# Kernel optimization log

Hardware: AMD Instinct MI355X
Metric: run time of the kernel (lower is better)

## Reference

```python
import jax, jax.numpy as jnp
import numpy as np

# config (matches init_kwargs)
B, L, Q = 4, 2048, 2048      # batch, memory_length, query_len
H, D = 16, 64                # heads, head_dim
E = H * D                    # hidden_dim = 1024
NB = 512                     # num_basis
SIGMAS = np.array([0.005, 0.01])
RIDGE = 0.5
CLAMP_MIN = 1e-4


def _build_basis():
    # torch.meshgrid(linspace(0,1,NB//2), sigmas) then flatten: mu repeated, sigma tiled
    mu = np.repeat(np.linspace(0.0, 1.0, NB // len(SIGMAS)), len(SIGMAS))
    sg = np.tile(SIGMAS, NB // len(SIGMAS))
    return mu, sg


def _build_G(mu, sg):
    # get_positions(L, padding=True), L even: 2L points in [-0.5+shift, 1.5-shift]
    shift = 1.0 / (2 * L)
    pos = np.linspace(-0.5 + shift, 1.5 - shift, 2 * L)
    # F[j, p] = N(pos_p; mu_j, sg_j)
    Fm = np.exp(-0.5 * ((pos[None, :] - mu[:, None]) / sg[:, None]) ** 2) / (sg[:, None] * np.sqrt(2 * np.pi))
    G = Fm.T @ np.linalg.inv(Fm @ Fm.T + RIDGE * np.eye(NB))  # [2L, NB]
    return G[L // 2:-(L // 2)]  # [L, NB]


def setup_inputs() -> dict:
    key = jax.random.key(0)
    ks = jax.random.split(key, 8)
    mu, sg = _build_basis()
    G = _build_G(mu, sg)
    s_e = 1.0 / np.sqrt(E)
    s_n = 1.0 / np.sqrt(NB)
    return {
        "k": jax.random.normal(ks[0], (B, L, E), jnp.float32),
        "q": jax.random.normal(ks[1], (B, Q, E), jnp.float32),
        "Wq": jax.random.normal(ks[2], (E, E), jnp.float32) * s_e,
        "Wk": jax.random.normal(ks[3], (E, E), jnp.float32) * s_e,
        "Wv": jax.random.normal(ks[4], (E, E), jnp.float32) * s_e,
        "Wo": jax.random.normal(ks[5], (E, E), jnp.float32) * s_e,
        "w_mu": jax.random.normal(ks[6], (NB,), jnp.float32) * s_n,
        "w_sigma": jax.random.normal(ks[7], (NB,), jnp.float32) * s_n,
        "Gs": jnp.asarray(G, jnp.float32),
        "basis_mu": jnp.asarray(mu, jnp.float32),
        "basis_sigma": jnp.asarray(sg, jnp.float32),
    }


def reference(k, q, Wq, Wk, Wv, Wo, w_mu, w_sigma, Gs, basis_mu, basis_sigma):
    # continuous compression of the memory: B_mat[b,n,e] = sum_l k[b,l,e] * Gs[l,n]
    Bm = jnp.einsum('ble,ln->bne', k, Gs)  # [B, NB, E]
    keys = (Bm @ Wk.T).reshape(B, NB, H, D).transpose(0, 2, 1, 3)   # [B,H,NB,D]
    vals = (Bm @ Wv.T).reshape(B, NB, H, D).transpose(0, 2, 1, 3)   # [B,H,NB,D]
    qry = (q @ Wq.T).reshape(B, Q, H, D).transpose(0, 2, 1, 3)      # [B,H,Q,D]
    # scores over basis functions
    scores = jnp.einsum('bhqd,bhnd->bhqn', qry, keys) / jnp.sqrt(jnp.float32(D))
    # affine heads -> Gaussian attention density parameters per query
    mu_q = jax.nn.sigmoid(scores @ w_mu)[..., None]                         # [B,H,Q,1]
    sig2 = jnp.clip(jax.nn.softplus(scores @ w_sigma), CLAMP_MIN)[..., None]  # [B,H,Q,1]
    # continuous softmax closed form: r_j = N(mu_q; basis_mu_j, sig2 + basis_sigma_j^2)
    var = sig2 + basis_sigma ** 2                                           # [B,H,Q,NB]
    r = jnp.exp(-0.5 * (mu_q - basis_mu) ** 2 / var) / jnp.sqrt(2.0 * jnp.pi * var)
    ctx = jnp.einsum('bhqn,bhnd->bhqd', r, vals)                            # [B,H,Q,D]
    ctx = ctx.transpose(0, 2, 1, 3).reshape(B, Q, E)
    return ctx @ Wo.T
```

## Files before the change

kernel.cpp:

```cpp
#include <hip/hip_runtime.h>

#define BB 4
#define LL 2048
#define QQ 2048
#define HH 16
#define DD 64
#define EE 1024
#define NB 512

typedef __attribute__((ext_vector_type(8))) short bf16x8;
typedef __attribute__((ext_vector_type(4))) float f32x4;

__device__ inline ushort bf16_rne(float f) {
  uint u = __float_as_uint(f);
  return (ushort)((u + 0x7fffu + ((u >> 16) & 1u)) >> 16);
}
__device__ inline float bf16_f(ushort h) { return __uint_as_float((uint)h << 16); }
__device__ inline void hilo(float x, ushort& h, ushort& l) {
  h = bf16_rne(x);
  l = bf16_rne(x - bf16_f(h));
}

__device__ inline void cvt8_pack(const float* a, uint4& ph, uint4& pl) {
  ushort h[8], l[8];
  #pragma unroll
  for (int j = 0; j < 8; j++) hilo(a[j], h[j], l[j]);
  ph = make_uint4((uint)h[0] | ((uint)h[1] << 16), (uint)h[2] | ((uint)h[3] << 16),
                  (uint)h[4] | ((uint)h[5] << 16), (uint)h[6] | ((uint)h[7] << 16));
  pl = make_uint4((uint)l[0] | ((uint)l[1] << 16), (uint)l[2] | ((uint)l[3] << 16),
                  (uint)l[4] | ((uint)l[5] << 16), (uint)l[6] | ((uint)l[7] << 16));
}

__global__ __launch_bounds__(256) void cvt_hilo(
    const float* __restrict__ x, ushort* __restrict__ hi, ushort* __restrict__ lo, long n)
{
  long i0 = ((long)blockIdx.x * 256 + threadIdx.x) * 8;
  long stride = (long)gridDim.x * 2048;
  for (long i = i0; i < n; i += stride) {
    float a[8];
    *(float4*)&a[0] = *(const float4*)&x[i];
    *(float4*)&a[4] = *(const float4*)&x[i + 4];
    uint4 ph, pl;
    cvt8_pack(a, ph, pl);
    *(uint4*)&hi[i] = ph;
    *(uint4*)&lo[i] = pl;
  }
}

__global__ __launch_bounds__(256) void cvt_hiloT(
    const float* __restrict__ x, ushort* __restrict__ hiT, ushort* __restrict__ loT,
    int R, int C, long zIn, long zOut)
{
  x += (long)blockIdx.z * zIn; hiT += (long)blockIdx.z * zOut; loT += (long)blockIdx.z * zOut;
  __shared__ float tile[32][33];
  const int t = threadIdx.x;
  const long r0 = (long)blockIdx.y * 32, c0 = (long)blockIdx.x * 32;
  {
    int row = t >> 3, c4 = t & 7;
    float4 v = *(const float4*)&x[(r0 + row) * C + c0 + c4 * 4];
    tile[row][c4*4+0] = v.x; tile[row][c4*4+1] = v.y;
    tile[row][c4*4+2] = v.z; tile[row][c4*4+3] = v.w;
  }
  __syncthreads();
  {
    int col = t >> 3, r4 = t & 7;
    ushort h[4], l[4];
    #pragma unroll
    for (int j = 0; j < 4; j++) hilo(tile[r4 * 4 + j][col], h[j], l[j]);
    uint2 ph = make_uint2((uint)h[0] | ((uint)h[1] << 16), (uint)h[2] | ((uint)h[3] << 16));
    uint2 pl = make_uint2((uint)l[0] | ((uint)l[1] << 16), (uint)l[2] | ((uint)l[3] << 16));
    long o = (c0 + col) * (long)R + r0 + r4 * 4;
    *(uint2*)&hiT[o] = ph;
    *(uint2*)&loT[o] = pl;
  }
}

__global__ __launch_bounds__(256) void add_pairs(
    float* __restrict__ dst, long dstStride,
    const float* __restrict__ src, long srcPairStride, long n)
{
  float* d = dst + (long)blockIdx.z * dstStride;
  const float* s0 = src + (long)blockIdx.z * srcPairStride;
  const float* s1 = s0 + n;
  long i0 = ((long)blockIdx.x * 256 + threadIdx.x) * 4;
  long stride = (long)gridDim.x * 1024;
  for (long i = i0; i < n; i += stride) {
    float4 a = *(const float4*)&s0[i];
    float4 b = *(const float4*)&s1[i];
    a.x += b.x; a.y += b.y; a.z += b.z; a.w += b.w;
    *(float4*)&d[i] = a;
  }
}


__global__ __launch_bounds__(256) void gemm_nt128(
    const float* __restrict__ A, const float* __restrict__ B, float* __restrict__ C,
    int N, int K, long sA, long sB, long sC, int NS, int Kc)
{
  const int z = blockIdx.z;
  const int b = z / NS, ks = z - b * NS;
  A += (long)b * sA + (long)ks * Kc;
  B += (long)b * sB + (long)ks * Kc;
  C += (long)z * sC;
  __shared__ float As[32][132], Bs[32][132];
  const int t = threadIdx.x;
  const int tx = t & 15, ty = t >> 4;
  const long m0 = (long)blockIdx.y * 128, n0 = (long)blockIdx.x * 128;
  float acc[8][8] = {};
  for (int k0 = 0; k0 < Kc; k0 += 32) {
    #pragma unroll
    for (int i = 0; i < 4; i++) {
      int f = t + i * 256;
      int r = f >> 3, k4 = f & 7;
      float4 va = *(const float4*)&A[(m0 + r) * K + k0 + k4 * 4];
      As[k4*4+0][r] = va.x; As[k4*4+1][r] = va.y; As[k4*4+2][r] = va.z; As[k4*4+3][r] = va.w;
      float4 vb = *(const float4*)&B[(n0 + r) * K + k0 + k4 * 4];
      Bs[k4*4+0][r] = vb.x; Bs[k4*4+1][r] = vb.y; Bs[k4*4+2][r] = vb.z; Bs[k4*4+3][r] = vb.w;
    }
    __syncthreads();
    #pragma unroll
    for (int kk = 0; kk < 32; kk++) {
      float4 a0 = *(const float4*)&As[kk][ty*8];
      float4 a1 = *(const float4*)&As[kk][ty*8+4];
      float4 b0 = *(const float4*)&Bs[kk][tx*8];
      float4 b1 = *(const float4*)&Bs[kk][tx*8+4];
      float ar[8] = {a0.x,a0.y,a0.z,a0.w,a1.x,a1.y,a1.z,a1.w};
      float br[8] = {b0.x,b0.y,b0.z,b0.w,b1.x,b1.y,b1.z,b1.w};
      #pragma unroll
      for (int i = 0; i < 8; i++)
        #pragma unroll
        for (int j = 0; j < 8; j++)
          acc[i][j] += ar[i] * br[j];
    }
    __syncthreads();
  }
  #pragma unroll
  for (int i = 0; i < 8; i++) {
    float4 o0 = make_float4(acc[i][0], acc[i][1], acc[i][2], acc[i][3]);
    float4 o1 = make_float4(acc[i][4], acc[i][5], acc[i][6], acc[i][7]);
    *(float4*)&C[(m0 + ty*8 + i) * N + n0 + tx*8    ] = o0;
    *(float4*)&C[(m0 + ty*8 + i) * N + n0 + tx*8 + 4] = o1;
  }
}

__global__ __launch_bounds__(256) void gemm_tn128(
    const float* __restrict__ A, const float* __restrict__ B, float* __restrict__ C,
    int M, int N, long sA, long sB, long sC, int NS, int Kc)
{
  const int z = blockIdx.z;
  const int b = z / NS, ks = z - b * NS;
  A += (long)b * sA + (long)ks * Kc * M;
  B += (long)b * sB + (long)ks * Kc * N;
  C += (long)z * sC;
  __shared__ float As[32][132], Bs[32][132];
  const int t = threadIdx.x;
  const int tx = t & 15, ty = t >> 4;
  const long m0 = (long)blockIdx.y * 128, n0 = (long)blockIdx.x * 128;
  float acc[8][8] = {};
  for (int k0 = 0; k0 < Kc; k0 += 32) {
    #pragma unroll
    for (int i = 0; i < 4; i++) {
      int f = t + i * 256;
      int r = f >> 5, c4 = f & 31;
      *(float4*)&As[r][c4 * 4] = *(const float4*)&A[(long)(k0 + r) * M + m0 + c4 * 4];
      *(float4*)&Bs[r][c4 * 4] = *(const float4*)&B[(long)(k0 + r) * N + n0 + c4 * 4];
    }
    __syncthreads();
    #pragma unroll
    for (int kk = 0; kk < 32; kk++) {
      float4 a0 = *(const float4*)&As[kk][ty*8];
      float4 a1 = *(const float4*)&As[kk][ty*8+4];
      float4 b0 = *(const float4*)&Bs[kk][tx*8];
      float4 b1 = *(const float4*)&Bs[kk][tx*8+4];
      float ar[8] = {a0.x,a0.y,a0.z,a0.w,a1.x,a1.y,a1.z,a1.w};
      float br[8] = {b0.x,b0.y,b0.z,b0.w,b1.x,b1.y,b1.z,b1.w};
      #pragma unroll
      for (int i = 0; i < 8; i++)
        #pragma unroll
        for (int j = 0; j < 8; j++)
          acc[i][j] += ar[i] * br[j];
    }
    __syncthreads();
  }
  #pragma unroll
  for (int i = 0; i < 8; i++) {
    float4 o0 = make_float4(acc[i][0], acc[i][1], acc[i][2], acc[i][3]);
    float4 o1 = make_float4(acc[i][4], acc[i][5], acc[i][6], acc[i][7]);
    *(float4*)&C[(m0 + ty*8 + i) * N + n0 + tx*8    ] = o0;
    *(float4*)&C[(m0 + ty*8 + i) * N + n0 + tx*8 + 4] = o1;
  }
}

__global__ __launch_bounds__(256) void gemm_nt64(
    const float* __restrict__ A, const float* __restrict__ B, float* __restrict__ C,
    int M, int N, int K, long sA, long sB, long sC)
{
  A += (long)blockIdx.z * sA; B += (long)blockIdx.z * sB; C += (long)blockIdx.z * sC;
  __shared__ float As[32][68], Bs[32][68];
  const int t = threadIdx.x;
  const int tx = t & 15, ty = t >> 4;
  const int m0 = blockIdx.y * 64, n0 = blockIdx.x * 64;
  float acc[4][4] = {};
  for (int k0 = 0; k0 < K; k0 += 32) {
    #pragma unroll
    for (int i = 0; i < 2; i++) {
      int f = t + i * 256;
      int r = f >> 3, k4 = f & 7;
      float4 va = *(const float4*)&A[(long)(m0 + r) * K + k0 + k4 * 4];
      As[k4*4+0][r] = va.x; As[k4*4+1][r] = va.y; As[k4*4+2][r] = va.z; As[k4*4+3][r] = va.w;
      float4 vb = *(const float4*)&B[(long)(n0 + r) * K + k0 + k4 * 4];
      Bs[k4*4+0][r] = vb.x; Bs[k4*4+1][r] = vb.y; Bs[k4*4+2][r] = vb.z; Bs[k4*4+3][r] = vb.w;
    }
    __syncthreads();
    #pragma unroll
    for (int kk = 0; kk < 32; kk++) {
      float4 a4 = *(const float4*)&As[kk][ty * 4];
      float4 b4 = *(const float4*)&Bs[kk][tx * 4];
      float ar[4] = {a4.x, a4.y, a4.z, a4.w};
      float br[4] = {b4.x, b4.y, b4.z, b4.w};
      #pragma unroll
      for (int i = 0; i < 4; i++)
        #pragma unroll
        for (int j = 0; j < 4; j++)
          acc[i][j] += ar[i] * br[j];
    }
    __syncthreads();
  }
  #pragma unroll
  for (int i = 0; i < 4; i++) {
    float4 o = make_float4(acc[i][0], acc[i][1], acc[i][2], acc[i][3]);
    *(float4*)&C[(long)(m0 + ty*4 + i) * N + n0 + tx*4] = o;
  }
}


__global__ __launch_bounds__(256) void gemm_nt128_b3(
    const ushort* __restrict__ Ah, const ushort* __restrict__ Al,
    const ushort* __restrict__ Bh, const ushort* __restrict__ Bl,
    float* __restrict__ C, int N, int K, long sA, long sC, int NS, int Kc)
{
  const int z = blockIdx.z;
  const int zb = z / NS, ks = z - zb * NS;
  Ah += (long)zb * sA + (long)ks * Kc;
  Al += (long)zb * sA + (long)ks * Kc;
  Bh += (long)ks * Kc;
  Bl += (long)ks * Kc;
  C  += (long)z * sC;
  __shared__ ushort AhS[4096], AlS[4096], BhS[4096], BlS[4096];
  const int t = threadIdx.x;
  const int l = t & 63, w = t >> 6;
  const long m0 = (long)blockIdx.y * 128, n0 = (long)blockIdx.x * 128;
  const int frA = (w & 1) * 4;
  const int frB = (w >> 1) * 4;
  f32x4 acc[4][4] = {};
  for (int k0 = 0; k0 < Kc; k0 += 32) {
    #pragma unroll
    for (int p = 0; p < 2; p++) {
      int t2 = t + p * 256;
      int row = t2 >> 2, kq = t2 & 3;
      long goff = (m0 + row) * (long)K + k0 + kq * 8;
      long gofB = (n0 + row) * (long)K + k0 + kq * 8;
      int dst = (row >> 4) * 512 + ((row & 15) + 16 * kq) * 8;
      *(uint4*)&AhS[dst] = *(const uint4*)(Ah + goff);
      *(uint4*)&AlS[dst] = *(const uint4*)(Al + goff);
      *(uint4*)&BhS[dst] = *(const uint4*)(Bh + gofB);
      *(uint4*)&BlS[dst] = *(const uint4*)(Bl + gofB);
    }
    __syncthreads();
    bf16x8 ah[4], al[4], bh[4], bl[4];
    #pragma unroll
    for (int i = 0; i < 4; i++) {
      ah[i] = *(const bf16x8*)&AhS[(frA + i) * 512 + l * 8];
      al[i] = *(const bf16x8*)&AlS[(frA + i) * 512 + l * 8];
      bh[i] = *(const bf16x8*)&BhS[(frB + i) * 512 + l * 8];
      bl[i] = *(const bf16x8*)&BlS[(frB + i) * 512 + l * 8];
    }
    #pragma unroll
    for (int i = 0; i < 4; i++)
      #pragma unroll
      for (int j = 0; j < 4; j++) {
        acc[i][j] = __builtin_amdgcn_mfma_f32_16x16x32_bf16(ah[i], bh[j], acc[i][j], 0, 0, 0);
        acc[i][j] = __builtin_amdgcn_mfma_f32_16x16x32_bf16(ah[i], bl[j], acc[i][j], 0, 0, 0);
        acc[i][j] = __builtin_amdgcn_mfma_f32_16x16x32_bf16(al[i], bh[j], acc[i][j], 0, 0, 0);
      }
    __syncthreads();
  }
  const long rbase = m0 + (w & 1) * 64 + (l >> 4) * 4;
  const int  cbase = (int)n0 + (w >> 1) * 64 + (l & 15);
  #pragma unroll
  for (int i = 0; i < 4; i++)
    #pragma unroll
    for (int j = 0; j < 4; j++)
      #pragma unroll
      for (int r = 0; r < 4; r++)
        C[(rbase + i * 16 + r) * N + cbase + j * 16] = acc[i][j][r];
}

__global__ __launch_bounds__(256) void gemm_nt64x128_b3(
    const ushort* __restrict__ Ah, const ushort* __restrict__ Al,
    const ushort* __restrict__ Bh, const ushort* __restrict__ Bl,
    float* __restrict__ C, int N, int K, long sB, long sC)
{
  const int z = blockIdx.z;
  Bh += (long)z * sB; Bl += (long)z * sB; C += (long)z * sC;
  __shared__ ushort AhS[2048], AlS[2048], BhS[4096], BlS[4096];
  const int t = threadIdx.x;
  const int l = t & 63, w = t >> 6;
  const long m0 = (long)blockIdx.y * 64, n0 = (long)blockIdx.x * 128;
  const int wm = w & 1, wn = w >> 1;
  f32x4 acc[2][4] = {};
  for (int k0 = 0; k0 < K; k0 += 32) {
    {
      int row = t >> 2, kq = t & 3;
      long goff = (m0 + row) * (long)K + k0 + kq * 8;
      int dst = (row >> 4) * 512 + ((row & 15) + 16 * kq) * 8;
      *(uint4*)&AhS[dst] = *(const uint4*)(Ah + goff);
      *(uint4*)&AlS[dst] = *(const uint4*)(Al + goff);
    }
    #pragma unroll
    for (int p = 0; p < 2; p++) {
      int t2 = t + p * 256;
      int row = t2 >> 2, kq = t2 & 3;
      long gofB = (n0 + row) * (long)K + k0 + kq * 8;
      int dst = (row >> 4) * 512 + ((row & 15) + 16 * kq) * 8;
      *(uint4*)&BhS[dst] = *(const uint4*)(Bh + gofB);
      *(uint4*)&BlS[dst] = *(const uint4*)(Bl + gofB);
    }
    __syncthreads();
    bf16x8 ah[2], al[2], bh[4], bl[4];
    #pragma unroll
    for (int i = 0; i < 2; i++) {
      ah[i] = *(const bf16x8*)&AhS[(wm * 2 + i) * 512 + l * 8];
      al[i] = *(const bf16x8*)&AlS[(wm * 2 + i) * 512 + l * 8];
    }
    #pragma unroll
    for (int j = 0; j < 4; j++) {
      bh[j] = *(const bf16x8*)&BhS[(wn * 4 + j) * 512 + l * 8];
      bl[j] = *(const bf16x8*)&BlS[(wn * 4 + j) * 512 + l * 8];
    }
    #pragma unroll
    for (int i = 0; i < 2; i++)
      #pragma unroll
      for (int j = 0; j < 4; j++) {
        acc[i][j] = __builtin_amdgcn_mfma_f32_16x16x32_bf16(ah[i], bh[j], acc[i][j], 0, 0, 0);
        acc[i][j] = __builtin_amdgcn_mfma_f32_16x16x32_bf16(ah[i], bl[j], acc[i][j], 0, 0, 0);
        acc[i][j] = __builtin_amdgcn_mfma_f32_16x16x32_bf16(al[i], bh[j], acc[i][j], 0, 0, 0);
      }
    __syncthreads();
  }
  const long rbase = m0 + wm * 32 + (l >> 4) * 4;
  const int  cbase = (int)n0 + wn * 64 + (l & 15);
  #pragma unroll
  for (int i = 0; i < 2; i++)
    #pragma unroll
    for (int j = 0; j < 4; j++)
      #pragma unroll
      for (int r = 0; r < 4; r++)
        C[(rbase + i * 16 + r) * N + cbase + j * 16] = acc[i][j][r];
}

__global__ __launch_bounds__(256) void cvt_valsT(
    const float* __restrict__ valsP, ushort* __restrict__ vTh, ushort* __restrict__ vTl,
    long slabStride)
{
  const int c = blockIdx.x, h = blockIdx.y, b = blockIdx.z;
  const int t = threadIdx.x;
  __shared__ float tile[32][68];
  const float* s0 = valsP + (long)(2 * b) * slabStride;
  const float* s1 = s0 + slabStride;
  {
    int r = t >> 3, c8 = (t & 7) * 8;
    long g = (long)(c * 32 + r) * EE + h * 64 + c8;
    float4 a0 = *(const float4*)&s0[g];     float4 b0 = *(const float4*)&s1[g];
    float4 a1 = *(const float4*)&s0[g + 4]; float4 b1 = *(const float4*)&s1[g + 4];
    a0.x += b0.x; a0.y += b0.y; a0.z += b0.z; a0.w += b0.w;
    a1.x += b1.x; a1.y += b1.y; a1.z += b1.z; a1.w += b1.w;
    *(float4*)&tile[r][c8] = a0;
    *(float4*)&tile[r][c8 + 4] = a1;
  }
  __syncthreads();
  const int f = t >> 6, l = t & 63;
  const int d = f * 16 + (l & 15), kq = l >> 4;
  float a[8];
  #pragma unroll
  for (int e = 0; e < 8; e++) a[e] = tile[kq * 8 + e][d];
  uint4 ph, pl;
  cvt8_pack(a, ph, pl);
  long obase = (((long)(b * HH + h) * 16 + c) * 2048) + (long)t * 8;
  *(uint4*)&vTh[obase] = ph;
  *(uint4*)&vTl[obase] = pl;
}

__global__ __launch_bounds__(256) void nb_ctx_mf(
    const ushort* __restrict__ vTh, const ushort* __restrict__ vTl,
    const float* __restrict__ muq, const float* __restrict__ sg2,
    const float* __restrict__ bmu, const float* __restrict__ bsg,
    ushort* __restrict__ ctxh, ushort* __restrict__ ctxl,
    long sMu, long sC)
{
  const int h = blockIdx.y, b = blockIdx.z;
  const long q0 = (long)blockIdx.x * 128;
  const int t = threadIdx.x;
  const int l = t & 63, w = t >> 6, wm = w & 1, wn = w >> 1;
  __shared__ ushort AhS[4096], AlS[4096];
  __shared__ ushort BhS[2048], BlS[2048];
  __shared__ float mu_s[128], s2_s[128], bm_s[NB], bv_s[NB];
  const float* muqb = muq + (long)b * sMu;
  const float* sg2b = sg2 + (long)b * sMu;
  if (t < 128) {
    mu_s[t] = muqb[(long)h * QQ + q0 + t];
    s2_s[t] = sg2b[(long)h * QQ + q0 + t];
  }
  for (int i = t; i < NB; i += 256) {
    bm_s[i] = bmu[i];
    float x = bsg[i];
    bv_s[i] = x * x;
  }
  __syncthreads();
  const ushort* vThb = vTh + ((long)(b * HH + h) * 16) * 2048;
  const ushort* vTlb = vTl + ((long)(b * HH + h) * 16) * 2048;
  f32x4 acc[4][2] = {};
  for (int c = 0; c < 16; c++) {
    ((uint4*)BhS)[t] = ((const uint4*)(vThb + c * 2048))[t];
    ((uint4*)BlS)[t] = ((const uint4*)(vTlb + c * 2048))[t];
    #pragma unroll
    for (int p = 0; p < 2; p++) {
      int s = t + p * 256;
      int lf = s & 63;
      int q = ((s >> 6) << 4) + (lf & 15);
      int nb = c * 32 + (lf >> 4) * 8;
      float m = mu_s[q], s2 = s2_s[q];
      float a[8];
      #pragma unroll
      for (int e = 0; e < 8; e++) {
        float v = s2 + bv_s[nb + e];
        float d = m - bm_s[nb + e];
        float rv = __builtin_amdgcn_rcpf(v);
        a[e] = __expf(d * d * rv * -0.5f) * __builtin_amdgcn_rsqf(v * 6.2831853071795865f);
      }
      uint4 ph, pl;
      cvt8_pack(a, ph, pl);
      *(uint4*)&AhS[s * 8] = ph;
      *(uint4*)&AlS[s * 8] = pl;
    }
    __syncthreads();
    bf16x8 bhf[2], blf[2];
    #pragma unroll
    for (int j = 0; j < 2; j++) {
      bhf[j] = *(const bf16x8*)&BhS[(wn * 2 + j) * 512 + l * 8];
      blf[j] = *(const bf16x8*)&BlS[(wn * 2 + j) * 512 + l * 8];
    }
    #pragma unroll
    for (int i = 0; i < 4; i++) {
      bf16x8 ah = *(const bf16x8*)&AhS[(wm * 4 + i) * 512 + l * 8];
      bf16x8 al = *(const bf16x8*)&AlS[(wm * 4 + i) * 512 + l * 8];
      #pragma unroll
      for (int j = 0; j < 2; j++) {
        acc[i][j] = __builtin_amdgcn_mfma_f32_16x16x32_bf16(ah, bhf[j], acc[i][j], 0, 0, 0);
        acc[i][j] = __builtin_amdgcn_mfma_f32_16x16x32_bf16(ah, blf[j], acc[i][j], 0, 0, 0);
        acc[i][j] = __builtin_amdgcn_mfma_f32_16x16x32_bf16(al, bhf[j], acc[i][j], 0, 0, 0);
      }
    }
    __syncthreads();
  }
  ushort* ch = ctxh + (long)b * sC;
  ushort* cl = ctxl + (long)b * sC;
  const long rbase = q0 + wm * 64 + (l >> 4) * 4;
  const int  cbase = h * 64 + wn * 32 + (l & 15);
  #pragma unroll
  for (int i = 0; i < 4; i++)
    #pragma unroll
    for (int j = 0; j < 2; j++)
      #pragma unroll
      for (int r = 0; r < 4; r++) {
        long off = (rbase + i * 16 + r) * EE + cbase + j * 16;
        ushort hb, lb;
        hilo(acc[i][j][r], hb, lb);
        ch[off] = hb;
        cl[off] = lb;
      }
}

__global__ __launch_bounds__(256) void nb_uvec(
    const float* __restrict__ Bm, const float* __restrict__ wmu, const float* __restrict__ wsg,
    float* __restrict__ ump, float* __restrict__ usp, long sBm, long sU)
{
  Bm += (long)blockIdx.z * sBm; ump += (long)blockIdx.z * sU; usp += (long)blockIdx.z * sU;
  const int e = blockIdx.x * 256 + threadIdx.x;
  const int c = blockIdx.y;
  float am = 0.f, as = 0.f;
  #pragma unroll 8
  for (int n = c * 64; n < c * 64 + 64; n++) {
    float bv = Bm[(long)n * EE + e];
    am += wmu[n] * bv;
    as += wsg[n] * bv;
  }
  ump[(long)c * EE + e] = am;
  usp[(long)c * EE + e] = as;
}

__global__ __launch_bounds__(256) void nb_kw(
    const float* __restrict__ Wk, const float* __restrict__ ump, const float* __restrict__ usp,
    float* __restrict__ kwm, float* __restrict__ kws, long sU, long sK)
{
  ump += (long)blockIdx.z * sU; usp += (long)blockIdx.z * sU;
  kwm += (long)blockIdx.z * sK; kws += (long)blockIdx.z * sK;
  __shared__ float pm[256], ps[256];
  const int e = blockIdx.x, t = threadIdx.x;
  const float* row = Wk + (long)e * EE;
  float am = 0.f, as = 0.f;
  for (int i = t; i < EE; i += 256) {
    float um = 0.f, us = 0.f;
    #pragma unroll
    for (int c = 0; c < 8; c++) { um += ump[(long)c * EE + i]; us += usp[(long)c * EE + i]; }
    float w = row[i];
    am += w * um;
    as += w * us;
  }
  pm[t] = am; ps[t] = as;
  __syncthreads();
  for (int s = 128; s > 0; s >>= 1) {
    if (t < s) { pm[t] += pm[t + s]; ps[t] += ps[t + s]; }
    __syncthreads();
  }
  if (t == 0) { kwm[e] = pm[0]; kws[e] = ps[0]; }
}

__global__ __launch_bounds__(256) void nb_amas(
    const float* __restrict__ Wq, const float* __restrict__ kwm, const float* __restrict__ kws,
    float* __restrict__ AmAs, long sK, long sAm)
{
  kwm += (long)blockIdx.z * sK; kws += (long)blockIdx.z * sK;
  AmAs += (long)blockIdx.z * sAm;
  __shared__ float km[64], ks[64];
  const int t = threadIdx.x;
  const int h = blockIdx.y;
  const int e = blockIdx.x * 256 + t;
  if (t < 64) { km[t] = kwm[h * 64 + t]; ks[t] = kws[h * 64 + t]; }
  __syncthreads();
  float am = 0.f, as = 0.f;
  #pragma unroll 8
  for (int d = 0; d < 64; d++) {
    float w = Wq[(long)(h * 64 + d) * EE + e];
    am += km[d] * w;
    as += ks[d] * w;
  }
  AmAs[(long)e * 32 + h]      = am;
  AmAs[(long)e * 32 + 16 + h] = as;
}

__global__ __launch_bounds__(256) void nb_musig(
    const float* __restrict__ qb, const float* __restrict__ AmAs,
    float* __restrict__ muq, float* __restrict__ sg2, long sQ, long sAm, long sMu)
{
  qb += (long)blockIdx.z * sQ; AmAs += (long)blockIdx.z * sAm;
  muq += (long)blockIdx.z * sMu; sg2 += (long)blockIdx.z * sMu;
  __shared__ float qs[EE];
  __shared__ float part[8][32];
  const int t = threadIdx.x, qrow = blockIdx.x;
  for (int i = t; i < EE; i += 256) qs[i] = qb[(long)qrow * EE + i];
  __syncthreads();
  const int o = t & 31, ch = t >> 5;
  float acc = 0.f;
  const int e0 = ch * 128;
  #pragma unroll 8
  for (int i = 0; i < 128; i++) {
    int e = e0 + i;
    acc += qs[e] * AmAs[(long)e * 32 + o];
  }
  part[ch][o] = acc;
  __syncthreads();
  if (t < 32) {
    float s = 0.f;
    #pragma unroll
    for (int c = 0; c < 8; c++) s += part[c][o];
    s *= 0.125f;
    if (o < 16) {
      muq[(long)o * QQ + qrow] = 1.f / (1.f + expf(-s));
    } else {
      float sp = (s > 20.f) ? s : log1pf(expf(s));
      sg2[(long)(o - 16) * QQ + qrow] = fmaxf(sp, 1e-4f);
    }
  }
}

__global__ __launch_bounds__(128) void nb_ctx128(
    const float* __restrict__ vals, const float* __restrict__ muq, const float* __restrict__ sg2,
    const float* __restrict__ bmu,  const float* __restrict__ bsg, float* __restrict__ ctx,
    long sV, long sMu, long sC)
{
  vals += (long)blockIdx.z * sV; ctx += (long)blockIdx.z * sC;
  muq += (long)blockIdx.z * sMu; sg2 += (long)blockIdx.z * sMu;
  __shared__ float As[32][132], Bs[32][68];
  __shared__ __align__(16) float mu_s[128], s2_s[128];
  const int t = threadIdx.x;
  const int tx = t & 7, ty = t >> 3;
  const long q0 = (long)blockIdx.x * 128;
  const int h = blockIdx.y;
  mu_s[t] = muq[(long)h * QQ + q0 + t];
  s2_s[t] = sg2[(long)h * QQ + q0 + t];
  __syncthreads();
  float acc[8][8] = {};
  for (int n0 = 0; n0 < NB; n0 += 32) {
    #pragma unroll
    for (int i = 0; i < 4; i++) {
      int f = t + i * 128;
      int r = f >> 4, c4 = f & 15;
      *(float4*)&Bs[r][c4 * 4] = *(const float4*)&vals[(long)(n0 + r) * EE + h * 64 + c4 * 4];
    }
    #pragma unroll
    for (int i = 0; i < 8; i++) {
      int idx = t + i * 128;
      int n = idx >> 5, qg = idx & 31;
      float bm = bmu[n0 + n], bs = bsg[n0 + n];
      float bs2 = bs * bs;
      float4 m4 = *(const float4*)&mu_s[qg * 4];
      float4 s4 = *(const float4*)&s2_s[qg * 4];
      float4 rr;
      {
        float v0 = s4.x + bs2, d0 = m4.x - bm;
        float v1 = s4.y + bs2, d1 = m4.y - bm;
        float v2 = s4.z + bs2, d2 = m4.z - bm;
        float v3 = s4.w + bs2, d3 = m4.w - bm;
        float r0 = __builtin_amdgcn_rcpf(v0), r1 = __builtin_amdgcn_rcpf(v1);
        float r2 = __builtin_amdgcn_rcpf(v2), r3 = __builtin_amdgcn_rcpf(v3);
        rr.x = __expf(d0 * d0 * r0 * -0.5f) * __builtin_amdgcn_rsqf(v0 * 6.2831853071795865f);
        rr.y = __expf(d1 * d1 * r1 * -0.5f) * __builtin_amdgcn_rsqf(v1 * 6.2831853071795865f);
        rr.z = __expf(d2 * d2 * r2 * -0.5f) * __builtin_amdgcn_rsqf(v2 * 6.2831853071795865f);
        rr.w = __expf(d3 * d3 * r3 * -0.5f) * __builtin_amdgcn_rsqf(v3 * 6.2831853071795865f);
      }
      *(float4*)&As[n][qg * 4] = rr;
    }
    __syncthreads();
    #pragma unroll
    for (int kk = 0; kk < 32; kk++) {
      float4 a0 = *(const float4*)&As[kk][ty*8];
      float4 a1 = *(const float4*)&As[kk][ty*8+4];
      float4 b0 = *(const float4*)&Bs[kk][tx*8];
      float4 b1 = *(const float4*)&Bs[kk][tx*8+4];
      float ar[8] = {a0.x,a0.y,a0.z,a0.w,a1.x,a1.y,a1.z,a1.w};
      float br[8] = {b0.x,b0.y,b0.z,b0.w,b1.x,b1.y,b1.z,b1.w};
      #pragma unroll
      for (int i = 0; i < 8; i++)
        #pragma unroll
        for (int j = 0; j < 8; j++)
          acc[i][j] += ar[i] * br[j];
    }
    __syncthreads();
  }
  #pragma unroll
  for (int i = 0; i < 8; i++) {
    float4 o0 = make_float4(acc[i][0], acc[i][1], acc[i][2], acc[i][3]);
    float4 o1 = make_float4(acc[i][4], acc[i][5], acc[i][6], acc[i][7]);
    *(float4*)&ctx[(q0 + ty*8 + i) * EE + h * 64 + tx*8    ] = o0;
    *(float4*)&ctx[(q0 + ty*8 + i) * EE + h * 64 + tx*8 + 4] = o1;
  }
}

extern "C" void kernel_launch(void* const* d_in, const int* in_sizes, int n_in,
                              void* d_out, int out_size, void* d_ws, size_t ws_size,
                              hipStream_t stream) {
  const float* k   = (const float*)d_in[0];
  const float* q   = (const float*)d_in[1];
  const float* Wq  = (const float*)d_in[2];
  const float* Wk  = (const float*)d_in[3];
  const float* Wv  = (const float*)d_in[4];
  const float* Wo  = (const float*)d_in[5];
  const float* wmu = (const float*)d_in[6];
  const float* wsg = (const float*)d_in[7];
  const float* Gs  = (const float*)d_in[8];
  const float* bmu = (const float*)d_in[9];
  const float* bsg = (const float*)d_in[10];
  float* out = (float*)d_out;
  char* ws = (char*)d_ws;

  const long sBm = (long)NB * EE;
  const long sU  = 8L * EE;
  const long sK  = EE;
  const long sAm = 32L * EE;
  const long sMu = (long)HH * QQ;
  const long sQ  = (long)QQ * EE;

  if (ws_size >= (50u << 20)) {
    ushort* kTh  = (ushort*)(ws + 0);
    ushort* kTl  = (ushort*)(ws + (16u << 20));
    ushort* GsTh = (ushort*)(ws + (32u << 20));
    ushort* GsTl = (ushort*)(ws + (34u << 20));
    float*  Bm4  = (float*)(ws + (40u << 20));
    ushort* Bmh  = (ushort*)(ws + 0);
    ushort* Bml  = (ushort*)(ws + (4u << 20));
    ushort* Wvh  = (ushort*)(ws + (8u << 20));
    ushort* Wvl  = (ushort*)(ws + (10u << 20));
    float*  valsP= (float*)(ws + (16u << 20));
    ushort* vTh  = (ushort*)(ws + (32u << 20));
    ushort* vTl  = (ushort*)(ws + (36u << 20));
    ushort* Woh  = (ushort*)(ws + (40u << 20));
    ushort* Wol  = (ushort*)(ws + (42u << 20));
    ushort* ctxh = (ushort*)(ws + 0);
    ushort* ctxl = (ushort*)(ws + (16u << 20));
    char*  sm    = ws + (48u << 20);
    float* ump4  = (float*)(sm);
    float* usp4  = (float*)(sm + (128u << 10));
    float* kwm4  = (float*)(sm + (256u << 10));
    float* kws4  = (float*)(sm + (272u << 10));
    float* AmAs4 = (float*)(sm + (288u << 10));
    float* muq4  = (float*)(sm + (800u << 10));
    float* sg24  = (float*)(sm + (1312u << 10));

    cvt_hiloT<<<dim3(NB/32, LL/32, 1),  256, 0, stream>>>(Gs, GsTh, GsTl, LL, NB, 0L, 0L);
    cvt_hiloT<<<dim3(EE/32, LL/32, BB), 256, 0, stream>>>(k, kTh, kTl, LL, EE,
                                                          (long)LL*EE, (long)LL*EE);
    gemm_nt64x128_b3<<<dim3(EE/128, NB/64, BB), 256, 0, stream>>>(
        GsTh, GsTl, kTh, kTl, Bm4, EE, LL, (long)LL*EE, sBm);
    nb_uvec  <<<dim3(EE/256, 8, BB),  256, 0, stream>>>(Bm4, wmu, wsg, ump4, usp4, sBm, sU);
    nb_kw    <<<dim3(EE, 1, BB),      256, 0, stream>>>(Wk, ump4, usp4, kwm4, kws4, sU, sK);
    nb_amas  <<<dim3(EE/256, HH, BB), 256, 0, stream>>>(Wq, kwm4, kws4, AmAs4, sK, sAm);
    nb_musig <<<dim3(QQ, 1, BB),      256, 0, stream>>>(q, AmAs4, muq4, sg24, sQ, sAm, sMu);
    cvt_hilo<<<dim3(256), 256, 0, stream>>>(Bm4, Bmh, Bml, (long)BB * sBm);
    cvt_hilo<<<dim3(256), 256, 0, stream>>>(Wv, Wvh, Wvl, (long)EE * EE);
    gemm_nt128_b3<<<dim3(EE/128, NB/128, BB*2), 256, 0, stream>>>(
        Bmh, Bml, Wvh, Wvl, valsP, EE, EE, sBm, sBm, 2, EE/2);
    cvt_valsT<<<dim3(16, HH, BB), 256, 0, stream>>>(valsP, vTh, vTl, sBm);
    cvt_hilo<<<dim3(256), 256, 0, stream>>>(Wo, Woh, Wol, (long)EE * EE);
    nb_ctx_mf<<<dim3(QQ/128, HH, BB), 256, 0, stream>>>(
        vTh, vTl, muq4, sg24, bmu, bsg, ctxh, ctxl, sMu, sQ);
    gemm_nt128_b3<<<dim3(EE/128, QQ/128, BB), 256, 0, stream>>>(
        ctxh, ctxl, Woh, Wol, out, EE, EE, sQ, sQ, 1, EE);
  } else {
    float* BmP   = (float*)(ws + 0);
    float* ctxS  = (float*)(ws + 0);
    float* vals4 = (float*)(ws + (16u << 20));
    char*  sm    = ws + (24u << 20);
    float* ump4  = (float*)(sm);
    float* usp4  = (float*)(sm + (128u << 10));
    float* kwm4  = (float*)(sm + (256u << 10));
    float* kws4  = (float*)(sm + (272u << 10));
    float* AmAs4 = (float*)(sm + (288u << 10));
    float* muq4  = (float*)(sm + (800u << 10));
    float* sg24  = (float*)(sm + (1312u << 10));

    gemm_tn128<<<dim3(EE/128, NB/128, BB*2), 256, 0, stream>>>(
        Gs, k, BmP, NB, EE, 0L, (long)LL*EE, sBm, 2, LL/2);
    add_pairs<<<dim3(256, 1, BB), 256, 0, stream>>>(BmP, 2*sBm, BmP, 2*sBm, sBm);
    gemm_nt128<<<dim3(EE/128, NB/128, BB), 256, 0, stream>>>(
        BmP, Wv, vals4, EE, EE, 2*sBm, 0L, sBm, 1, EE);
    nb_uvec  <<<dim3(EE/256, 8, BB),  256, 0, stream>>>(BmP, wmu, wsg, ump4, usp4, 2*sBm, sU);
    nb_kw    <<<dim3(EE, 1, BB),      256, 0, stream>>>(Wk, ump4, usp4, kwm4, kws4, sU, sK);
    nb_amas  <<<dim3(EE/256, HH, BB), 256, 0, stream>>>(Wq, kwm4, kws4, AmAs4, sK, sAm);
    nb_musig <<<dim3(QQ, 1, BB),      256, 0, stream>>>(q, AmAs4, muq4, sg24, sQ, sAm, sMu);
    for (int b = 0; b < BB; b++) {
      nb_ctx128<<<dim3(QQ/128, HH, 1), 128, 0, stream>>>(
          vals4 + (long)b*sBm, muq4 + (long)b*sMu, sg24 + (long)b*sMu,
          bmu, bsg, ctxS, 0L, 0L, 0L);
      gemm_nt64<<<dim3(EE/64, QQ/64, 1), 256, 0, stream>>>(
          ctxS, Wo, out + (long)b*sQ, QQ, EE, EE, 0L, 0L, 0L);
    }
  }
  (void)in_sizes; (void)n_in; (void)out_size;
}
```

Measured before the change: 435.0 us.

## Swizzle GEMM LDS layout, batch musig rows, merge Wv/Wo conversion launches

Three independent changes. The LDS tiles in both split-bf16 GEMM kernels are now stored with an XOR swizzle on the row index, keyed by the k-quarter, and fragment reads use the matching swizzled offset, so LDS bank conflicts on stores and reads should drop. The mu/sigma projection kernel now processes 8 query rows per block, so each AmAs load serves eight rows instead of one, at the cost of 32KB of shared memory per block. The two separate Wv and Wo hi/lo conversion launches are merged into one two-slice launch to save a kernel launch.

```diff
diff --git a/kernel.cpp b/kernel.cpp
--- a/kernel.cpp
+++ b/kernel.cpp
@@ -47,6 +47,26 @@
   }
 }
 
+__global__ __launch_bounds__(256) void cvt_hilo2(
+    const float* __restrict__ x0, ushort* __restrict__ h0, ushort* __restrict__ l0,
+    const float* __restrict__ x1, ushort* __restrict__ h1, ushort* __restrict__ l1, long n)
+{
+  const float* x = blockIdx.y ? x1 : x0;
+  ushort* hi = blockIdx.y ? h1 : h0;
+  ushort* lo = blockIdx.y ? l1 : l0;
+  long i0 = ((long)blockIdx.x * 256 + threadIdx.x) * 8;
+  long stride = (long)gridDim.x * 2048;
+  for (long i = i0; i < n; i += stride) {
+    float a[8];
+    *(float4*)&a[0] = *(const float4*)&x[i];
+    *(float4*)&a[4] = *(const float4*)&x[i + 4];
+    uint4 ph, pl;
+    cvt8_pack(a, ph, pl);
+    *(uint4*)&hi[i] = ph;
+    *(uint4*)&lo[i] = pl;
+  }
+}
+
 __global__ __launch_bounds__(256) void cvt_hiloT(
     const float* __restrict__ x, ushort* __restrict__ hiT, ushort* __restrict__ loT,
     int R, int C, long zIn, long zOut)
@@ -252,6 +272,7 @@
   const long m0 = (long)blockIdx.y * 128, n0 = (long)blockIdx.x * 128;
   const int frA = (w & 1) * 4;
   const int frB = (w >> 1) * 4;
+  const int rs = ((((l & 15) ^ ((l >> 4) << 2)) + 16 * (l >> 4))) * 8;
   f32x4 acc[4][4] = {};
   for (int k0 = 0; k0 < Kc; k0 += 32) {
     #pragma unroll
@@ -260,7 +281,7 @@
       int row = t2 >> 2, kq = t2 & 3;
       long goff = (m0 + row) * (long)K + k0 + kq * 8;
       long gofB = (n0 + row) * (long)K + k0 + kq * 8;
-      int dst = (row >> 4) * 512 + ((row & 15) + 16 * kq) * 8;
+      int dst = (row >> 4) * 512 + ((((row & 15) ^ (kq << 2)) + 16 * kq)) * 8;
       *(uint4*)&AhS[dst] = *(const uint4*)(Ah + goff);
       *(uint4*)&AlS[dst] = *(const uint4*)(Al + goff);
       *(uint4*)&BhS[dst] = *(const uint4*)(Bh + gofB);
@@ -270,10 +291,10 @@
     bf16x8 ah[4], al[4], bh[4], bl[4];
     #pragma unroll
     for (int i = 0; i < 4; i++) {
-      ah[i] = *(const bf16x8*)&AhS[(frA + i) * 512 + l * 8];
-      al[i] = *(const bf16x8*)&AlS[(frA + i) * 512 + l * 8];
-      bh[i] = *(const bf16x8*)&BhS[(frB + i) * 512 + l * 8];
-      bl[i] = *(const bf16x8*)&BlS[(frB + i) * 512 + l * 8];
+      ah[i] = *(const bf16x8*)&AhS[(frA + i) * 512 + rs];
+      al[i] = *(const bf16x8*)&AlS[(frA + i) * 512 + rs];
+      bh[i] = *(const bf16x8*)&BhS[(frB + i) * 512 + rs];
+      bl[i] = *(const bf16x8*)&BlS[(frB + i) * 512 + rs];
     }
     #pragma unroll
     for (int i = 0; i < 4; i++)
@@ -308,12 +329,13 @@
   const int l = t & 63, w = t >> 6;
   const long m0 = (long)blockIdx.y * 64, n0 = (long)blockIdx.x * 128;
   const int wm = w & 1, wn = w >> 1;
+  const int rs = ((((l & 15) ^ ((l >> 4) << 2)) + 16 * (l >> 4))) * 8;
   f32x4 acc[2][4] = {};
   for (int k0 = 0; k0 < K; k0 += 32) {
     {
       int row = t >> 2, kq = t & 3;
       long goff = (m0 + row) * (long)K + k0 + kq * 8;
-      int dst = (row >> 4) * 512 + ((row & 15) + 16 * kq) * 8;
+      int dst = (row >> 4) * 512 + ((((row & 15) ^ (kq << 2)) + 16 * kq)) * 8;
       *(uint4*)&AhS[dst] = *(const uint4*)(Ah + goff);
       *(uint4*)&AlS[dst] = *(const uint4*)(Al + goff);
     }
@@ -322,7 +344,7 @@
       int t2 = t + p * 256;
       int row = t2 >> 2, kq = t2 & 3;
       long gofB = (n0 + row) * (long)K + k0 + kq * 8;
-      int dst = (row >> 4) * 512 + ((row & 15) + 16 * kq) * 8;
+      int dst = (row >> 4) * 512 + ((((row & 15) ^ (kq << 2)) + 16 * kq)) * 8;
       *(uint4*)&BhS[dst] = *(const uint4*)(Bh + gofB);
       *(uint4*)&BlS[dst] = *(const uint4*)(Bl + gofB);
     }
@@ -330,13 +352,13 @@
     bf16x8 ah[2], al[2], bh[4], bl[4];
     #pragma unroll
     for (int i = 0; i < 2; i++) {
-      ah[i] = *(const bf16x8*)&AhS[(wm * 2 + i) * 512 + l * 8];
-      al[i] = *(const bf16x8*)&AlS[(wm * 2 + i) * 512 + l * 8];
+      ah[i] = *(const bf16x8*)&AhS[(wm * 2 + i) * 512 + rs];
+      al[i] = *(const bf16x8*)&AlS[(wm * 2 + i) * 512 + rs];
     }
     #pragma unroll
     for (int j = 0; j < 4; j++) {
-      bh[j] = *(const bf16x8*)&BhS[(wn * 4 + j) * 512 + l * 8];
-      bl[j] = *(const bf16x8*)&BlS[(wn * 4 + j) * 512 + l * 8];
+      bh[j] = *(const bf16x8*)&BhS[(wn * 4 + j) * 512 + rs];
+      bl[j] = *(const bf16x8*)&BlS[(wn * 4 + j) * 512 + rs];
     }
     #pragma unroll
     for (int i = 0; i < 2; i++)
@@ -547,6 +569,33 @@
   }
   AmAs[(long)e * 32 + h]      = am;
   AmAs[(long)e * 32 + 16 + h] = as;
+}
+
+__global__ __launch_bounds__(256) void nb_musig8(
+    const float* __restrict__ qb, const float* __restrict__ AmAs,
+    float* __restrict__ muq, float* __restrict__ sg2, long sQ, long sAm, long sMu)
+{
+  qb += (long)blockIdx.z * sQ; AmAs += (long)blockIdx.z * sAm;
+  muq += (long)blockIdx.z * sMu; sg2 += (long)blockIdx.z * sMu;
+  __shared__ float qs[8 * EE];
+  const int t = threadIdx.x;
+  const long q0 = (long)blockIdx.x * 8;
+  for (int i = t * 4; i < 8 * EE; i += 1024)
+    *(float4*)&qs[i] = *(const float4*)&qb[q0 * EE + i];
+  __syncthreads();
+  const int o = t & 31, row = t >> 5;
+  const float* qr = qs + row * EE;
+  float acc = 0.f;
+  #pragma unroll 8
+  for (int e = 0; e < EE; e++)
+    acc += qr[e] * AmAs[(long)e * 32 + o];
+  float s = acc * 0.125f;
+  if (o < 16) {
+    muq[(long)o * QQ + q0 + row] = 1.f / (1.f + expf(-s));
+  } else {
+    float sp = (s > 20.f) ? s : log1pf(expf(s));
+    sg2[(long)(o - 16) * QQ + q0 + row] = fmaxf(sp, 1e-4f);
+  }
 }
 
 __global__ __launch_bounds__(256) void nb_musig(
@@ -715,13 +764,12 @@
     nb_uvec  <<<dim3(EE/256, 8, BB),  256, 0, stream>>>(Bm4, wmu, wsg, ump4, usp4, sBm, sU);
     nb_kw    <<<dim3(EE, 1, BB),      256, 0, stream>>>(Wk, ump4, usp4, kwm4, kws4, sU, sK);
     nb_amas  <<<dim3(EE/256, HH, BB), 256, 0, stream>>>(Wq, kwm4, kws4, AmAs4, sK, sAm);
-    nb_musig <<<dim3(QQ, 1, BB),      256, 0, stream>>>(q, AmAs4, muq4, sg24, sQ, sAm, sMu);
+    nb_musig8<<<dim3(QQ/8, 1, BB),    256, 0, stream>>>(q, AmAs4, muq4, sg24, sQ, sAm, sMu);
     cvt_hilo<<<dim3(256), 256, 0, stream>>>(Bm4, Bmh, Bml, (long)BB * sBm);
-    cvt_hilo<<<dim3(256), 256, 0, stream>>>(Wv, Wvh, Wvl, (long)EE * EE);
+    cvt_hilo2<<<dim3(128, 2), 256, 0, stream>>>(Wv, Wvh, Wvl, Wo, Woh, Wol, (long)EE * EE);
     gemm_nt128_b3<<<dim3(EE/128, NB/128, BB*2), 256, 0, stream>>>(
         Bmh, Bml, Wvh, Wvl, valsP, EE, EE, sBm, sBm, 2, EE/2);
     cvt_valsT<<<dim3(16, HH, BB), 256, 0, stream>>>(valsP, vTh, vTl, sBm);
-    cvt_hilo<<<dim3(256), 256, 0, stream>>>(Wo, Woh, Wol, (long)EE * EE);
     nb_ctx_mf<<<dim3(QQ/128, HH, BB), 256, 0, stream>>>(
         vTh, vTl, muq4, sg24, bmu, bsg, ctxh, ctxl, sMu, sQ);
     gemm_nt128_b3<<<dim3(EE/128, QQ/128, BB), 256, 0, stream>>>(
```

Result: faster. 422.3 us (-2.9%).
